# Performance work log

Measured on AMD Instinct MI355X. Metric: run time of the kernel, lower is better.

Reference implementation:

```python
import jax, jax.numpy as jnp
import numpy as np

DIM = 1024
NUM_ROT = 1024
BATCH = 65536


def setup_inputs() -> dict:
    key = jax.random.key(0)
    k1, k2 = jax.random.split(key)
    x = jax.random.normal(k1, (BATCH, DIM), dtype=jnp.float32)
    angles = jax.random.normal(k2, (NUM_ROT,), dtype=jnp.float32)
    return {"x": x, "angles": angles}


def reference(x, angles):
    # Sequential Givens rotations. out @ R.T with R[i,i]=R[j,j]=c, R[i,j]=-s, R[j,i]=s
    # is equivalent to: col_i' = c*col_i - s*col_j ; col_j' = s*col_i + c*col_j.
    dim = x.shape[-1]
    num_rot = angles.shape[0]
    ii = jnp.arange(num_rot, dtype=jnp.int32)          # pairs (i, (i+1)%dim)
    jj = (ii + 1) % dim

    def step(out, inp):
        theta, i, j = inp
        c, s = jnp.cos(theta), jnp.sin(theta)
        ci = out[:, i]
        cj = out[:, j]
        out = out.at[:, i].set(c * ci - s * cj)
        out = out.at[:, j].set(s * ci + c * cj)
        return out, None

    out, _ = jax.lax.scan(step, x, (angles, ii, jj))
    return out
```

## Files before the change

kernel.cpp:

```cpp
#include <hip/hip_runtime.h>

#define DIM   1024
#define LPR   32
#define SEG   (DIM / LPR)
#define SEG4  (SEG / 4)
#define ROWS_PER_BLOCK 8
#define WAVES_PER_BLOCK 4

typedef float f32x4 __attribute__((ext_vector_type(4)));

__global__ __launch_bounds__(256, 4)
void qll_kernel(const float* __restrict__ x,
                const float* __restrict__ angles,
                float* __restrict__ out,
                int batch)
{
    __shared__ float2 cs[DIM];
    __shared__ f32x4  stage[WAVES_PER_BLOCK][512];

    for (int j = threadIdx.x; j < DIM; j += blockDim.x) {
        float a = angles[j];
        cs[(j & 31) * LPR + (j >> 5)] = make_float2(cosf(a), sinf(a));
    }
    __syncthreads();

    const int tid  = threadIdx.x;
    const int l    = tid & 63;
    const int wave = tid >> 6;
    const int h    = (tid >> 5) & 1;
    const int t    = tid & 31;
    const int r0   = blockIdx.x * ROWS_PER_BLOCK + wave * 2;
    if (r0 + 2 > batch) return;

    const int swz_l = l ^ ((l >> 3) & 7);

    const f32x4* gin = reinterpret_cast<const f32x4*>(x) + (size_t)r0 * 256;
#pragma unroll
    for (int m = 0; m < 8; ++m) {
        __builtin_amdgcn_global_load_lds(
            (const __attribute__((address_space(1))) void*)(gin + m * 64 + swz_l),
            (__attribute__((address_space(3))) void*)(&stage[wave][m * 64]),
            16, 0, 0);
    }
    asm volatile("s_waitcnt vmcnt(0)" ::: "memory");
    __builtin_amdgcn_sched_barrier(0);

    float v[SEG];
#pragma unroll
    for (int e = 0; e < SEG4; ++e) {
        f32x4 q = stage[wave][h * 256 + t * 8 + (e ^ (t & 7))];
        v[4*e+0] = q.x; v[4*e+1] = q.y; v[4*e+2] = q.z; v[4*e+3] = q.w;
    }

    float v0row = __shfl(v[0], 0, LPR);
    float v1row = __shfl(v[1], 0, LPR);
    float vnext = __shfl_down(v[0], 1, LPR);

    float A = 1.f, B = 0.f;
#pragma unroll
    for (int i = 0; i < SEG - 1; ++i) {
        float2 w = cs[i * LPR + t];
        B = w.y * B + w.x * v[i + 1];
        A = w.y * A;
    }
    {
        float2 w = cs[(SEG - 1) * LPR + t];
        B = w.y * B + w.x * vnext;
        A = w.y * A;
    }

#pragma unroll
    for (int d = 1; d < LPR; d <<= 1) {
        float pa = __shfl_up(A, d, LPR);
        float pb = __shfl_up(B, d, LPR);
        if (t >= d) { B = A * pb + B; A = A * pa; }
    }
    float ea = __shfl_up(A, 1, LPR);
    float eb = __shfl_up(B, 1, LPR);
    if (t == 0) { ea = 1.f; eb = 0.f; }
    float carry = ea * v0row + eb;

    float2 w0 = cs[0];
    float out0_prov = w0.x * v0row - w0.y * v1row;

#pragma unroll
    for (int i = 0; i < SEG - 1; ++i) {
        float2 w = cs[i * LPR + t];
        float vn = v[i + 1];
        float o  = w.x * carry - w.y * vn;
        carry    = w.y * carry + w.x * vn;
        v[i] = o;
    }
    {
        float2 w  = cs[(SEG - 1) * LPR + t];
        float vn  = (t == LPR - 1) ? out0_prov : vnext;
        float o   = w.x * carry - w.y * vn;
        float nc  = w.y * carry + w.x * vn;
        v[SEG - 1] = o;
        float out0_final = __shfl(nc, LPR - 1, LPR);
        if (t == 0) v[0] = out0_final;
    }

#pragma unroll
    for (int e = 0; e < SEG4; ++e) {
        f32x4 q = { v[4*e+0], v[4*e+1], v[4*e+2], v[4*e+3] };
        stage[wave][h * 256 + t * 8 + (e ^ (t & 7))] = q;
    }
    f32x4* gout = reinterpret_cast<f32x4*>(out) + (size_t)r0 * 256;
#pragma unroll
    for (int m = 0; m < 8; ++m) {
        f32x4 q = stage[wave][m * 64 + swz_l];
        __builtin_nontemporal_store(q, gout + m * 64 + l);
    }
}

extern "C" void kernel_launch(void* const* d_in, const int* in_sizes, int n_in,
                              void* d_out, int out_size, void* d_ws, size_t ws_size,
                              hipStream_t stream) {
    const float* x      = (const float*)d_in[0];
    const float* angles = (const float*)d_in[1];
    float* outp         = (float*)d_out;

    int batch = in_sizes[0] / DIM;
    int grid  = (batch + ROWS_PER_BLOCK - 1) / ROWS_PER_BLOCK;
    qll_kernel<<<grid, 256, 0, stream>>>(x, angles, outp, batch);
}
```

Before: 90.70 us.

## Map one row per 64-lane wave instead of two rows per wave

Each wave now processes a single row across all 64 lanes, so every lane holds 16 elements instead of 32. The angle table layout, LDS staging swizzle and segmented scan are reworked to match, and launch bounds rise to allow more blocks per CU. The aim is lower register pressure, higher occupancy and a shorter sequential loop per lane, paid for with one more scan step and more blocks in the grid.

```diff
diff --git a/kernel.cpp b/kernel.cpp
--- a/kernel.cpp
+++ b/kernel.cpp
@@ -1,45 +1,44 @@
 #include <hip/hip_runtime.h>
 
 #define DIM   1024
-#define LPR   32
+#define LPR   64
 #define SEG   (DIM / LPR)
 #define SEG4  (SEG / 4)
-#define ROWS_PER_BLOCK 8
+#define ROWS_PER_BLOCK 4
 #define WAVES_PER_BLOCK 4
 
 typedef float f32x4 __attribute__((ext_vector_type(4)));
 
-__global__ __launch_bounds__(256, 4)
+__global__ __launch_bounds__(256, 6)
 void qll_kernel(const float* __restrict__ x,
                 const float* __restrict__ angles,
                 float* __restrict__ out,
                 int batch)
 {
     __shared__ float2 cs[DIM];
-    __shared__ f32x4  stage[WAVES_PER_BLOCK][512];
+    __shared__ f32x4  stage[WAVES_PER_BLOCK][256];
 
-    for (int j = threadIdx.x; j < DIM; j += blockDim.x) {
+    for (int loc = threadIdx.x; loc < DIM; loc += blockDim.x) {
+        int j = ((loc & 63) << 4) | (loc >> 6);
         float a = angles[j];
-        cs[(j & 31) * LPR + (j >> 5)] = make_float2(cosf(a), sinf(a));
+        cs[loc] = make_float2(cosf(a), sinf(a));
     }
     __syncthreads();
 
     const int tid  = threadIdx.x;
     const int l    = tid & 63;
-    const int wave = tid >> 6;
-    const int h    = (tid >> 5) & 1;
-    const int t    = tid & 31;
-    const int r0   = blockIdx.x * ROWS_PER_BLOCK + wave * 2;
-    if (r0 + 2 > batch) return;
+    const int wv   = tid >> 6;
+    const int r0   = blockIdx.x * ROWS_PER_BLOCK + wv;
+    if (r0 >= batch) return;
 
-    const int swz_l = l ^ ((l >> 3) & 7);
+    const int swz_l = l ^ ((l >> 3) & 3);
 
     const f32x4* gin = reinterpret_cast<const f32x4*>(x) + (size_t)r0 * 256;
 #pragma unroll
-    for (int m = 0; m < 8; ++m) {
+    for (int m = 0; m < SEG4; ++m) {
         __builtin_amdgcn_global_load_lds(
             (const __attribute__((address_space(1))) void*)(gin + m * 64 + swz_l),
-            (__attribute__((address_space(3))) void*)(&stage[wave][m * 64]),
+            (__attribute__((address_space(3))) void*)(&stage[wv][m * 64]),
             16, 0, 0);
     }
     asm volatile("s_waitcnt vmcnt(0)" ::: "memory");
@@ -48,36 +47,36 @@
     float v[SEG];
 #pragma unroll
     for (int e = 0; e < SEG4; ++e) {
-        f32x4 q = stage[wave][h * 256 + t * 8 + (e ^ (t & 7))];
+        f32x4 q = stage[wv][l * 4 + (e ^ ((l >> 1) & 3))];
         v[4*e+0] = q.x; v[4*e+1] = q.y; v[4*e+2] = q.z; v[4*e+3] = q.w;
     }
 
-    float v0row = __shfl(v[0], 0, LPR);
-    float v1row = __shfl(v[1], 0, LPR);
-    float vnext = __shfl_down(v[0], 1, LPR);
+    float v0row = __shfl(v[0], 0);
+    float v1row = __shfl(v[1], 0);
+    float vnext = __shfl_down(v[0], 1);
 
     float A = 1.f, B = 0.f;
 #pragma unroll
     for (int i = 0; i < SEG - 1; ++i) {
-        float2 w = cs[i * LPR + t];
+        float2 w = cs[i * LPR + l];
         B = w.y * B + w.x * v[i + 1];
         A = w.y * A;
     }
     {
-        float2 w = cs[(SEG - 1) * LPR + t];
+        float2 w = cs[(SEG - 1) * LPR + l];
         B = w.y * B + w.x * vnext;
         A = w.y * A;
     }
 
 #pragma unroll
     for (int d = 1; d < LPR; d <<= 1) {
-        float pa = __shfl_up(A, d, LPR);
-        float pb = __shfl_up(B, d, LPR);
-        if (t >= d) { B = A * pb + B; A = A * pa; }
+        float pa = __shfl_up(A, d);
+        float pb = __shfl_up(B, d);
+        if (l >= d) { B = A * pb + B; A = A * pa; }
     }
-    float ea = __shfl_up(A, 1, LPR);
-    float eb = __shfl_up(B, 1, LPR);
-    if (t == 0) { ea = 1.f; eb = 0.f; }
+    float ea = __shfl_up(A, 1);
+    float eb = __shfl_up(B, 1);
+    if (l == 0) { ea = 1.f; eb = 0.f; }
     float carry = ea * v0row + eb;
 
     float2 w0 = cs[0];
@@ -85,31 +84,31 @@
 
 #pragma unroll
     for (int i = 0; i < SEG - 1; ++i) {
-        float2 w = cs[i * LPR + t];
+        float2 w = cs[i * LPR + l];
         float vn = v[i + 1];
         float o  = w.x * carry - w.y * vn;
         carry    = w.y * carry + w.x * vn;
         v[i] = o;
     }
     {
-        float2 w  = cs[(SEG - 1) * LPR + t];
-        float vn  = (t == LPR - 1) ? out0_prov : vnext;
+        float2 w  = cs[(SEG - 1) * LPR + l];
+        float vn  = (l == LPR - 1) ? out0_prov : vnext;
         float o   = w.x * carry - w.y * vn;
         float nc  = w.y * carry + w.x * vn;
         v[SEG - 1] = o;
-        float out0_final = __shfl(nc, LPR - 1, LPR);
-        if (t == 0) v[0] = out0_final;
+        float out0_final = __shfl(nc, LPR - 1);
+        if (l == 0) v[0] = out0_final;
     }
 
 #pragma unroll
     for (int e = 0; e < SEG4; ++e) {
         f32x4 q = { v[4*e+0], v[4*e+1], v[4*e+2], v[4*e+3] };
-        stage[wave][h * 256 + t * 8 + (e ^ (t & 7))] = q;
+        stage[wv][l * 4 + (e ^ ((l >> 1) & 3))] = q;
     }
     f32x4* gout = reinterpret_cast<f32x4*>(out) + (size_t)r0 * 256;
 #pragma unroll
-    for (int m = 0; m < 8; ++m) {
-        f32x4 q = stage[wave][m * 64 + swz_l];
+    for (int m = 0; m < SEG4; ++m) {
+        f32x4 q = stage[wv][m * 64 + swz_l];
         __builtin_nontemporal_store(q, gout + m * 64 + l);
     }
 }
```

Result: slower. 103.5 us (+14.1%).
